# Kernel tuning notes

Measured on AMD Instinct MI355X. Metric: run time of the kernel, lower is better.

Reference implementation:

```python
import jax, jax.numpy as jnp
import numpy as np
from jax import lax

B = 256

elu = jax.nn.elu

def conv2d(x, w, b=None, stride=1, pad=0):
    out = lax.conv_general_dilated(x, w, (stride, stride), [(pad, pad), (pad, pad)],
                                   dimension_numbers=('NCHW', 'OIHW', 'NCHW'))
    if b is not None:
        out = out + b[None, :, None, None]
    return out

def convT2d(x, w, b, stride, pad):
    k = w.shape[2]
    wt = jnp.flip(w, (2, 3)).transpose(1, 0, 2, 3)
    p = k - 1 - pad
    out = lax.conv_general_dilated(x, wt, (1, 1), [(p, p), (p, p)], lhs_dilation=(stride, stride),
                                   dimension_numbers=('NCHW', 'OIHW', 'NCHW'))
    return out + b[None, :, None, None]

def batchnorm(x, g, b, eps=1e-5):
    m = x.mean((0, 2, 3), keepdims=True)
    v = x.var((0, 2, 3), keepdims=True)
    return g[None, :, None, None] * (x - m) * lax.rsqrt(v + eps) + b[None, :, None, None]

def pool2(x, op):
    b, c, h, w = x.shape
    h2, w2 = (h // 2) * 2, (w // 2) * 2
    xr = x[:, :, :h2, :w2].reshape(b, c, h2 // 2, 2, w2 // 2, 2)
    return xr.max((3, 5)) if op == 'max' else xr.mean((3, 5))

def cubic(A, Bv, C, D, t):
    a = -0.5 * A + 1.5 * Bv - 1.5 * C + 0.5 * D
    b = A - 2.5 * Bv + 2.0 * C - 0.5 * D
    c = -0.5 * A + 0.5 * C
    return ((a * t + b) * t + c) * t + Bv

def bicubic_resize(x, nh, nw):
    b, h, w, c = x.shape
    fy = jnp.arange(nh, dtype=x.dtype) * ((h - 1) / max(nh - 1, 1))
    fx = jnp.arange(nw, dtype=x.dtype) * ((w - 1) / max(nw - 1, 1))
    y0 = jnp.floor(fy).astype(jnp.int32); ty = (fy - y0)[None, :, None, None]
    x0 = jnp.floor(fx).astype(jnp.int32); tx = (fx - x0)[None, None, :, None]
    rows = []
    for ky in (-1, 0, 1, 2):
        r = x[:, jnp.clip(y0 + ky, 0, h - 1)]
        cols = [r[:, :, jnp.clip(x0 + kx, 0, w - 1)] for kx in (-1, 0, 1, 2)]
        rows.append(cubic(cols[0], cols[1], cols[2], cols[3], tx))
    return cubic(rows[0], rows[1], rows[2], rows[3], ty)

def warp_bicubic(V, img):
    b, h, w, _ = V.shape
    gx = jnp.linspace(-1., 1., w)[None, None, :] + V[..., 0]
    gy = jnp.linspace(-1., 1., h)[None, :, None] + V[..., 1]
    ix = (gx + 1) * (w - 1) / 2
    iy = (gy + 1) * (h - 1) / 2
    x0 = jnp.floor(ix); y0 = jnp.floor(iy)
    tx = ix - x0; ty = iy - y0
    flat = img.reshape(b, h * w)
    def g(ky, kx):
        yi = jnp.clip(y0 + ky, 0, h - 1).astype(jnp.int32)
        xi = jnp.clip(x0 + kx, 0, w - 1).astype(jnp.int32)
        return jnp.take_along_axis(flat, (yi * w + xi).reshape(b, -1), 1).reshape(b, h, w)
    rows = [cubic(g(ky, -1), g(ky, 0), g(ky, 1), g(ky, 2), tx) for ky in (-1, 0, 1, 2)]
    return cubic(rows[0], rows[1], rows[2], rows[3], ty)[..., None]

def grid_sample_bilinear(img, gx, gy):
    b, h, w = img.shape
    ix = ((gx + 1) * w - 1) / 2
    iy = ((gy + 1) * h - 1) / 2
    x0 = jnp.floor(ix); y0 = jnp.floor(iy)
    tx = ix - x0; ty = iy - y0
    flat = img.reshape(b, h * w)
    def g(xi, yi):
        valid = (xi >= 0) & (xi <= w - 1) & (yi >= 0) & (yi <= h - 1)
        xc = jnp.clip(xi, 0, w - 1).astype(jnp.int32)
        yc = jnp.clip(yi, 0, h - 1).astype(jnp.int32)
        v = jnp.take_along_axis(flat, (yc * w + xc).reshape(b, -1), 1).reshape(b, h, w)
        return jnp.where(valid, v, 0.)
    return ((1 - tx) * (1 - ty) * g(x0, y0) + tx * (1 - ty) * g(x0 + 1, y0)
            + (1 - tx) * ty * g(x0, y0 + 1) + tx * ty * g(x0 + 1, y0 + 1))

def deform_conv(x, pw, pb, mw, mb, w):
    b, c, h, wd = x.shape
    N = 9
    off = conv2d(x, pw, pb, pad=1)
    m = jax.nn.sigmoid(conv2d(x, mw, mb, pad=1))
    r = jnp.array([-1., 0., 1.], x.dtype)
    pnx, pny = jnp.meshgrid(r, r, indexing='ij')
    pnx = pnx.reshape(-1); pny = pny.reshape(-1)
    p0x = jnp.arange(1, h + 1, dtype=x.dtype)[None, None, :, None]
    p0y = jnp.arange(1, wd + 1, dtype=x.dtype)[None, None, None, :]
    Hp, Wp = h + 2, wd + 2
    px = jnp.clip(p0x + pnx[None, :, None, None] + off[:, :N], 0, Hp - 1)
    py = jnp.clip(p0y + pny[None, :, None, None] + off[:, N:], 0, Wp - 1)
    fx = jnp.floor(px); fy = jnp.floor(py)
    x0 = jnp.clip(fx, 0, Hp - 1); y0 = jnp.clip(fy, 0, Wp - 1)
    x1_ = jnp.clip(fx + 1, 0, Hp - 1); y1_ = jnp.clip(fy + 1, 0, Wp - 1)
    g_lt = (1 + (x0 - px)) * (1 + (y0 - py))
    g_rb = (1 - (x1_ - px)) * (1 - (y1_ - py))
    g_lb = (1 + (x0 - px)) * (1 - (y1_ - py))
    g_rt = (1 - (x1_ - px)) * (1 + (y0 - py))
    xpad = jnp.pad(x, ((0, 0), (0, 0), (1, 1), (1, 1))).reshape(b, c, Hp * Wp)
    def gather(qx, qy):
        idx = (qx * Wp + qy).astype(jnp.int32).reshape(b, 1, -1)
        v = jnp.take_along_axis(xpad, jnp.broadcast_to(idx, (b, c, idx.shape[-1])), 2)
        return v.reshape(b, c, N, h, wd)
    v = (g_lt[:, None] * gather(x0, y0) + g_rb[:, None] * gather(x1_, y1_)
         + g_lb[:, None] * gather(x0, y1_) + g_rt[:, None] * gather(x1_, y0))
    v = v * m[:, None]
    v = v.reshape(b, c, 3, 3, h, wd).transpose(0, 1, 4, 2, 5, 3).reshape(b, c, h * 3, wd * 3)
    return conv2d(v, w, stride=3)

def stn(x, lw1, lb1, lw2, lb2, fw1, fb1, fw2, fb2):
    xs = jax.nn.relu(pool2(conv2d(x, lw1, lb1), 'max'))
    xs = jax.nn.relu(pool2(conv2d(xs, lw2, lb2), 'max'))
    xs = xs.reshape(xs.shape[0], -1)
    th = jax.nn.relu(xs @ fw1.T + fb1) @ fw2.T + fb2
    theta = th.reshape(-1, 2, 3)
    b, _, h, w = x.shape
    ys = (2 * jnp.arange(h) + 1) / h - 1
    xn = (2 * jnp.arange(w) + 1) / w - 1
    GX, GY = jnp.meshgrid(xn, ys, indexing='xy')
    gx = theta[:, 0, 0][:, None, None] * GX + theta[:, 0, 1][:, None, None] * GY + theta[:, 0, 2][:, None, None]
    gy = theta[:, 1, 0][:, None, None] * GX + theta[:, 1, 1][:, None, None] * GY + theta[:, 1, 2][:, None, None]
    warped = grid_sample_bilinear(x[:, 0], gx, gy)
    return jnp.stack([warped, x[:, 1]], 1)

def _forward(x1, loc1_w, loc1_b, loc2_w, loc2_b, fc1_w, fc1_b, fc2_w, fc2_b, conv1_w, conv1_b, bn1_g, bn1_b, dc2_pw, dc2_pb, dc2_mw, dc2_mb, dc2_w, bn2_g, bn2_b, conv3_w, conv3_b, bn3_g, bn3_b, dc41_pw, dc41_pb, dc41_mw, dc41_mb, dc41_w, bn41_g, bn41_b, conv4_w, conv4_b, conv4m_w, conv4m_b, conv3m_w, conv3m_b, conv2m_w, conv2m_b, conv1m_w, conv1m_b):
    _ = stn(x1, loc1_w, loc1_b, loc2_w, loc2_b, fc1_w, fc1_b, fc2_w, fc2_b)
    x = elu(batchnorm(conv2d(x1, conv1_w, conv1_b, pad=1), bn1_g, bn1_b))
    x = pool2(x, 'avg')
    x = elu(batchnorm(deform_conv(x, dc2_pw, dc2_pb, dc2_mw, dc2_mb, dc2_w), bn2_g, bn2_b))
    x = elu(batchnorm(conv2d(x, conv3_w, conv3_b, pad=1), bn3_g, bn3_b))
    x = pool2(x, 'avg')
    x = elu(batchnorm(deform_conv(x, dc41_pw, dc41_pb, dc41_mw, dc41_mb, dc41_w), bn41_g, bn41_b))
    x = conv2d(x, conv4_w, conv4_b, pad=1)
    dvf = bicubic_resize(x.transpose(0, 3, 2, 1), 7, 7)
    x = dvf.transpose(0, 3, 2, 1)
    x = convT2d(x, conv4m_w, conv4m_b, 2, 1)
    x = convT2d(x, conv3m_w, conv3m_b, 1, 0)
    x = elu(x)
    x = elu(convT2d(x, conv2m_w, conv2m_b, 2, 1))
    x = elu(convT2d(x, conv1m_w, conv1m_b, 1, 1))
    Vt = bicubic_resize(x.transpose(0, 3, 2, 1), 28, 28)
    return warp_bicubic(Vt, x1[:, 0])

def setup_inputs() -> dict:
    key = jax.random.key(0)
    ks = iter(jax.random.split(key, 64))
    def rn(shape, s=0.05):
        return jax.random.normal(next(ks), shape, jnp.float32) * s
    return dict(
        x1=jax.random.normal(next(ks), (B, 2, 28, 28), jnp.float32),
        loc1_w=rn((8, 2, 7, 7)), loc1_b=rn((8,)),
        loc2_w=rn((10, 8, 5, 5)), loc2_b=rn((10,)),
        fc1_w=rn((32, 90)), fc1_b=rn((32,)),
        fc2_w=jnp.zeros((6, 32), jnp.float32),
        fc2_b=jnp.array([1., 0., 0., 0., 1., 0.], jnp.float32),
        conv1_w=rn((64, 2, 3, 3)), conv1_b=rn((64,)),
        bn1_g=jnp.ones((64,), jnp.float32), bn1_b=jnp.zeros((64,), jnp.float32),
        dc2_pw=rn((18, 64, 3, 3)), dc2_pb=rn((18,)),
        dc2_mw=rn((9, 64, 3, 3)), dc2_mb=rn((9,)),
        dc2_w=rn((128, 64, 3, 3)),
        bn2_g=jnp.ones((128,), jnp.float32), bn2_b=jnp.zeros((128,), jnp.float32),
        conv3_w=rn((128, 128, 3, 3)), conv3_b=rn((128,)),
        bn3_g=jnp.ones((128,), jnp.float32), bn3_b=jnp.zeros((128,), jnp.float32),
        dc41_pw=rn((18, 128, 3, 3)), dc41_pb=rn((18,)),
        dc41_mw=rn((9, 128, 3, 3)), dc41_mb=rn((9,)),
        dc41_w=rn((64, 128, 3, 3)),
        bn41_g=jnp.ones((64,), jnp.float32), bn41_b=jnp.zeros((64,), jnp.float32),
        conv4_w=rn((2, 64, 3, 3)), conv4_b=rn((2,)),
        conv4m_w=rn((2, 128, 3, 3)), conv4m_b=rn((128,)),
        conv3m_w=rn((128, 64, 3, 3)), conv3m_b=rn((64,)),
        conv2m_w=rn((64, 32, 3, 3)), conv2m_b=rn((32,)),
        conv1m_w=rn((32, 2, 2, 2)), conv1m_b=rn((2,)),
    )

def reference(x1, loc1_w, loc1_b, loc2_w, loc2_b, fc1_w, fc1_b, fc2_w, fc2_b, conv1_w, conv1_b, bn1_g, bn1_b, dc2_pw, dc2_pb, dc2_mw, dc2_mb, dc2_w, bn2_g, bn2_b, conv3_w, conv3_b, bn3_g, bn3_b, dc41_pw, dc41_pb, dc41_mw, dc41_mb, dc41_w, bn41_g, bn41_b, conv4_w, conv4_b, conv4m_w, conv4m_b, conv3m_w, conv3m_b, conv2m_w, conv2m_b, conv1m_w, conv1m_b):
    return _forward(x1, loc1_w, loc1_b, loc2_w, loc2_b, fc1_w, fc1_b, fc2_w, fc2_b, conv1_w, conv1_b, bn1_g, bn1_b, dc2_pw, dc2_pb, dc2_mw, dc2_mb, dc2_w, bn2_g, bn2_b, conv3_w, conv3_b, bn3_g, bn3_b, dc41_pw, dc41_pb, dc41_mw, dc41_mb, dc41_w, bn41_g, bn41_b, conv4_w, conv4_b, conv4m_w, conv4m_b, conv3m_w, conv3m_b, conv2m_w, conv2m_b, conv1m_w, conv1m_b)
```

## Files before the change

### kernel.cpp

```cpp
#include <hip/hip_runtime.h>
#include <hip/hip_bf16.h>
#include <hip/hip_fp16.h>

__device__ __forceinline__ float eluf(float x){ return x > 0.f ? x : expm1f(x); }

typedef __attribute__((ext_vector_type(8))) short bf16x8;
typedef __attribute__((ext_vector_type(8))) _Float16 f16x8;
typedef __attribute__((ext_vector_type(4))) float f32x4;

__device__ __forceinline__ unsigned int bf16r(float f){
  unsigned int u = __float_as_uint(f);
  return (u + 0x7FFFu + ((u >> 16) & 1u)) >> 16;
}

__device__ __forceinline__ unsigned short f16b(float f){
  __half h = __float2half(f);
  return __half_as_ushort(h);
}

constexpr int pad_stride(int wp){
  int s = (wp + 3) & ~3;
  return (s % 8 == 0) ? s + 4 : s;
}

__global__ __launch_bounds__(256)
void conv1_stats(const float* __restrict__ in, const float* __restrict__ w,
                 const float* __restrict__ bias, float* __restrict__ part)
{
  constexpr int WPL = pad_stride(30);
  __shared__ __align__(16) float img[2][30*WPL];
  __shared__ float wl[2][8*9];
  __shared__ float sred[8], qred[8];
  const int b = blockIdx.x, gy = blockIdx.y, o0 = gy*8, t = threadIdx.x;
  const int ol = t & 7, y = t >> 3;
  if (t < 8){ sred[t] = 0.f; qred[t] = 0.f; }
  for (int idx = t; idx < 2*30*WPL; idx += 256) ((float*)img)[idx] = 0.f;
  __syncthreads();
  for (int idx = t; idx < 2*784; idx += 256){
    int cl = idx/784, r = idx%784;
    img[cl][(r/28 + 1)*WPL + (r%28) + 1] = in[((long long)b*2)*784 + idx];
  }
  if (t < 144){
    int cl = t/72, r = t%72;
    wl[cl][r] = w[(((long long)(o0 + r/9))*2 + cl)*9 + (r%9)];
  }
  __syncthreads();
  const bool active = (y < 28);
  float acc[28];
  #pragma unroll
  for (int x = 0; x < 28; x++) acc[x] = 0.f;
  if (active){
    for (int cl = 0; cl < 2; cl++){
      #pragma unroll
      for (int ky = 0; ky < 3; ky++){
        const float* row = &img[cl][(y+ky)*WPL];
        float rin[30];
        #pragma unroll
        for (int q = 0; q < 7; q++){
          float4 v = ((const float4*)row)[q];
          rin[4*q+0]=v.x; rin[4*q+1]=v.y; rin[4*q+2]=v.z; rin[4*q+3]=v.w;
        }
        rin[28] = row[28]; rin[29] = row[29];
        #pragma unroll
        for (int kx = 0; kx < 3; kx++){
          float wv = wl[cl][ol*9 + ky*3 + kx];
          #pragma unroll
          for (int x = 0; x < 28; x++) acc[x] += wv * rin[x+kx];
        }
      }
    }
  }
  const int og = o0 + ol;
  float sv = 0.f, qv = 0.f;
  if (active){
    float bv = bias[og];
    #pragma unroll
    for (int x = 0; x < 28; x++){
      float v = acc[x] + bv;
      sv += v; qv += v*v;
    }
  }
  #pragma unroll
  for (int d = 32; d >= 8; d >>= 1){
    sv += __shfl_down(sv, d);
    qv += __shfl_down(qv, d);
  }
  if ((t & 63) < 8){ atomicAdd(&sred[ol], sv); atomicAdd(&qred[ol], qv); }
  __syncthreads();
  if (t < 8){
    float* pp = part + ((long long)(b*8 + gy))*16;
    pp[t]     = sred[t];
    pp[t + 8] = qred[t];
  }
}

__global__ __launch_bounds__(256)
void conv1_reduce(const float* __restrict__ part, float* __restrict__ sum, float* __restrict__ sq)
{
  __shared__ float ss[256], qq[256];
  const int t = threadIdx.x;
  const int c = t & 63, seg = t >> 6;
  const int gy = c >> 3, ol = c & 7;
  float sv = 0.f, qv = 0.f;
  for (int b = seg*64; b < seg*64 + 64; b++){
    const float* pp = part + ((long long)(b*8 + gy))*16;
    sv += pp[ol];
    qv += pp[ol + 8];
  }
  ss[t] = sv; qq[t] = qv;
  __syncthreads();
  if (t < 64){
    sum[c] = ss[t] + ss[t+64] + ss[t+128] + ss[t+192];
    sq[c]  = qq[t] + qq[t+64] + qq[t+128] + qq[t+192];
  }
}

__global__ __launch_bounds__(256)
void conv1_pool(const float* __restrict__ in, const float* __restrict__ w,
                const float* __restrict__ bias, const float* __restrict__ g,
                const float* __restrict__ bb, const float* __restrict__ sum,
                const float* __restrict__ sq, float* __restrict__ out)
{
  constexpr int WPL = pad_stride(30);
  constexpr int PST = 197;
  __shared__ __align__(16) float img[2][30*WPL];
  __shared__ float wl[2][16*9];
  __shared__ float pout[16*PST];
  const int b = blockIdx.x, o0 = blockIdx.y*16, t = threadIdx.x;
  const int ol = t & 15, yp = t >> 4;
  for (int idx = t; idx < 2*30*WPL; idx += 256) ((float*)img)[idx] = 0.f;
  __syncthreads();
  for (int idx = t; idx < 2*784; idx += 256){
    int cl = idx/784, r = idx%784;
    img[cl][(r/28 + 1)*WPL + (r%28) + 1] = in[((long long)b*2)*784 + idx];
  }
  for (int idx = t; idx < 288; idx += 256){
    int cl = idx/144, r = idx%144;
    wl[cl][r] = w[(((long long)(o0 + r/9))*2 + cl)*9 + (r%9)];
  }
  __syncthreads();
  if (yp < 14){
    float accA[28], accB[28];
    #pragma unroll
    for (int x = 0; x < 28; x++){ accA[x] = 0.f; accB[x] = 0.f; }
    for (int cl = 0; cl < 2; cl++){
      #pragma unroll
      for (int ky = 0; ky < 3; ky++){
        const float* rowA = &img[cl][(2*yp+ky)*WPL];
        const float* rowB = rowA + WPL;
        float ra[30], rb[30];
        #pragma unroll
        for (int q = 0; q < 7; q++){
          float4 va = ((const float4*)rowA)[q];
          ra[4*q+0]=va.x; ra[4*q+1]=va.y; ra[4*q+2]=va.z; ra[4*q+3]=va.w;
          float4 vb = ((const float4*)rowB)[q];
          rb[4*q+0]=vb.x; rb[4*q+1]=vb.y; rb[4*q+2]=vb.z; rb[4*q+3]=vb.w;
        }
        ra[28]=rowA[28]; ra[29]=rowA[29];
        rb[28]=rowB[28]; rb[29]=rowB[29];
        #pragma unroll
        for (int kx = 0; kx < 3; kx++){
          float wv = wl[cl][ol*9 + ky*3 + kx];
          #pragma unroll
          for (int x = 0; x < 28; x++){
            accA[x] += wv * ra[x+kx];
            accB[x] += wv * rb[x+kx];
          }
        }
      }
    }
    const int og = o0 + ol;
    const float bv = bias[og];
    const float invN = 1.f/200704.f;
    float mean = sum[og]*invN;
    float var  = sq[og]*invN - mean*mean;
    float sc = g[og] * rsqrtf(var + 1e-5f);
    float sh = bb[og] - mean*sc;
    float* po = &pout[ol*PST + yp*14];
    #pragma unroll
    for (int xp = 0; xp < 14; xp++){
      float acc = eluf(sc*(accA[2*xp]   + bv) + sh);
      acc      += eluf(sc*(accA[2*xp+1] + bv) + sh);
      acc      += eluf(sc*(accB[2*xp]   + bv) + sh);
      acc      += eluf(sc*(accB[2*xp+1] + bv) + sh);
      po[xp] = acc * 0.25f;
    }
  }
  __syncthreads();
  float* gbase = out + ((long long)b*64 + o0)*196;
  for (int idx = t; idx < 3136; idx += 256)
    gbase[idx] = pout[(idx/196)*PST + idx%196];
}

template<int CIN,int H,int W,int NZ>
__global__ __launch_bounds__(256)
void offmask_tiled(const float* __restrict__ in, const float* __restrict__ pw,
                   const float* __restrict__ pb, const float* __restrict__ mw,
                   const float* __restrict__ mb, float* __restrict__ om)
{
  constexpr int Hz  = H/NZ;
  constexpr int HP  = Hz + 2;
  constexpr int WP  = W + 2;
  constexpr int WPL = pad_stride(WP);
  __shared__ __align__(16) float img[CIN*HP*WPL];
  const int b = blockIdx.x;
  const int z = blockIdx.y;
  const int t = threadIdx.x;
  for (int i = t; i < CIN*HP*WPL; i += 256) img[i] = 0.f;
  __syncthreads();
  const int base = z*Hz - 1;
  const int gy0  = (base < 0) ? 0 : base;
  const int gy1  = (z*Hz + Hz + 1 > H) ? H : z*Hz + Hz + 1;
  const int nrows = gy1 - gy0;
  for (int i = t; i < CIN*nrows*W; i += 256){
    int x = i % W; int r = i / W;
    int row = r % nrows; int c = r / nrows;
    int gy = gy0 + row;
    img[(c*HP + (gy - base))*WPL + (x+1)] = in[((long long)b*CIN + c)*(H*W) + gy*W + x];
  }
  __syncthreads();
  const int o  = t & 31;
  const int yl = t >> 5;
  const int y  = z*Hz + yl;
  if (o < 27 && yl < Hz && y < H){
    float acc[W];
    #pragma unroll
    for (int x = 0; x < W; x++) acc[x] = 0.f;
    const float* wsrc = (o < 18) ? (pw + (long long)o*CIN*9) : (mw + (long long)(o-18)*CIN*9);
    for (int c = 0; c < CIN; c++){
      const float* wc = wsrc + c*9;
      float4 wa = *(const float4*)wc;
      float4 wbv = *(const float4*)(wc+4);
      float w8 = wc[8];
      const float* rm = &img[(c*HP + yl  )*WPL];
      const float* r0 = &img[(c*HP + yl+1)*WPL];
      const float* rp = &img[(c*HP + yl+2)*WPL];
      #pragma unroll
      for (int x = 0; x < W; x++){
        acc[x] += wa.x*rm[x] + wa.y*rm[x+1] + wa.z*rm[x+2]
                + wa.w*r0[x] + wbv.x*r0[x+1] + wbv.y*r0[x+2]
                + wbv.z*rp[x] + wbv.w*rp[x+1] + w8*rp[x+2];
      }
    }
    float bv = (o < 18) ? pb[o] : mb[o-18];
    float* po = om + (((long long)b*27 + o)*H + y)*W;
    #pragma unroll
    for (int x = 0; x < W; x++){
      float v = acc[x] + bv;
      if (o >= 18) v = 1.f/(1.f + expf(-v));
      po[x] = v;
    }
  }
}

__global__ __launch_bounds__(256)
void conv4_tiled(const float* __restrict__ in, const float* __restrict__ w,
                 const float* __restrict__ bias, float* __restrict__ out)
{
  __shared__ __align__(16) float img[64*9*12];
  __shared__ float wl[1152];
  const int b = blockIdx.x, t = threadIdx.x;
  for (int i = t; i < 64*108; i += 256) img[i] = 0.f;
  __syncthreads();
  for (int i = t; i < 64*49; i += 256){
    int px = i % 49, c = i / 49;
    img[(c*9 + px/7 + 1)*12 + (px%7) + 1] = in[((long long)b*64 + c)*49 + px];
  }
  for (int i = t; i < 1152; i += 256) wl[i] = w[i];
  __syncthreads();
  const int o  = t >> 7;
  const int px = t & 127;
  if (px < 49){
    int y = px/7, x = px%7;
    float acc = bias[o];
    const float* wo = &wl[o*576];
    for (int c = 0; c < 64; c++){
      const float* rm = &img[(c*9 + y)*12 + x];
      const float* r0 = rm + 12;
      const float* rp = rm + 24;
      const float* wc = wo + c*9;
      acc += wc[0]*rm[0]+wc[1]*rm[1]+wc[2]*rm[2]
           + wc[3]*r0[0]+wc[4]*r0[1]+wc[5]*r0[2]
           + wc[6]*rp[0]+wc[7]*rp[1]+wc[8]*rp[2];
    }
    out[((long long)b*2 + o)*49 + px] = acc;
  }
}

__global__ void wconv3_bf16_kernel(const float* __restrict__ w, unsigned short* __restrict__ wb)
{
  int idx = blockIdx.x*256 + threadIdx.x;
  if (idx >= 147456) return;
  int kk = idx >> 14;
  int r  = idx & 16383;
  int o  = r >> 7, c = r & 127;
  wb[idx] = (unsigned short)bf16r(w[((long long)o*128 + c)*9 + kk]);
}

__global__ void bn2_pack_kernel(const float* __restrict__ a2, const float* __restrict__ g,
                                const float* __restrict__ bb, const float* __restrict__ sum,
                                const float* __restrict__ sq, unsigned int* __restrict__ a2b)
{
  int idx = blockIdx.x*256 + threadIdx.x;
  if (idx >= 4194304) return;
  int c2 = idx & 31; int r = idx >> 5;
  int hp = r & 255; r >>= 8;
  int ch = r & 1; int b = r >> 1;
  int row = hp >> 4, col = hp & 15;
  unsigned val = 0u;
  if (row >= 1 && row <= 14 && col >= 1 && col <= 14){
    int px = (row-1)*14 + (col-1);
    int c = ch*64 + 2*c2;
    const float invN = 1.f/50176.f;
    float m0 = sum[c]*invN,     m1 = sum[c+1]*invN;
    float v0 = sq[c]*invN - m0*m0, v1 = sq[c+1]*invN - m1*m1;
    float sc0 = g[c]*rsqrtf(v0 + 1e-5f), sc1 = g[c+1]*rsqrtf(v1 + 1e-5f);
    float sh0 = bb[c] - m0*sc0, sh1 = bb[c+1] - m1*sc1;
    float x0 = a2[((long long)b*128 + c)*196 + px];
    float x1 = a2[((long long)b*128 + c + 1)*196 + px];
    float e0 = eluf(sc0*x0 + sh0), e1 = eluf(sc1*x1 + sh1);
    val = bf16r(e0) | (bf16r(e1) << 16);
  }
  a2b[idx] = val;
}

__global__ __launch_bounds__(256)
void conv3_mfma2(const unsigned short* __restrict__ a2b, const unsigned short* __restrict__ wb,
                 const float* __restrict__ bias, float* __restrict__ out,
                 float* __restrict__ sum, float* __restrict__ sq)
{
  constexpr int RS = 72;
  __shared__ __align__(16) unsigned short img[256*RS];
  __shared__ float sred[64], qred[64];
  const int b  = blockIdx.x;
  const int o0 = blockIdx.y * 64;
  const int t  = threadIdx.x;
  const int lane = t & 63, wv = t >> 6;
  const int l15 = lane & 15, q = lane >> 4;
  const int ntile = (wv == 0) ? 4 : 3;
  if (t < 64){ sred[t] = 0.f; qred[t] = 0.f; }
  int rbase[4];
  #pragma unroll
  for (int ti = 0; ti < 4; ti++){
    int px = (wv + ti*4)*16 + l15;
    int pxe = px < 196 ? px : 195;
    rbase[ti] = (pxe/14)*16 + (pxe%14);
  }
  f32x4 acc[4][4];
  #pragma unroll
  for (int og = 0; og < 4; og++)
    #pragma unroll
    for (int ti = 0; ti < 4; ti++) acc[og][ti] = (f32x4){0.f,0.f,0.f,0.f};
  for (int ch = 0; ch < 2; ch++){
    __syncthreads();
    const unsigned short* src = a2b + ((long long)(b*2 + ch))*16384;
    for (int it = t; it < 2048; it += 256){
      int r = it >> 3, j = it & 7;
      uint4 v = *(const uint4*)(src + r*64 + j*8);
      *(uint4*)&img[r*RS + j*8] = v;
    }
    __syncthreads();
    #pragma unroll
    for (int kk = 0; kk < 9; kk++){
      int dh = (kk/3)*16 + (kk%3);
      #pragma unroll
      for (int ks = 0; ks < 2; ks++){
        bf16x8 bf[4];
        #pragma unroll
        for (int ti = 0; ti < 4; ti++)
          if (ti < ntile)
            bf[ti] = *(const bf16x8*)&img[(rbase[ti]+dh)*RS + ks*32 + q*8];
        #pragma unroll
        for (int og = 0; og < 4; og++){
          const unsigned short* wp = wb + (((long long)kk*128 + o0 + og*16 + l15)*128 + ch*64 + ks*32 + q*8);
          bf16x8 af = *(const bf16x8*)wp;
          #pragma unroll
          for (int ti = 0; ti < 4; ti++)
            if (ti < ntile)
              acc[og][ti] = __builtin_amdgcn_mfma_f32_16x16x32_bf16(af, bf[ti], acc[og][ti], 0, 0, 0);
        }
      }
    }
  }
  float svl[4][4], qvl[4][4];
  #pragma unroll
  for (int og = 0; og < 4; og++)
    #pragma unroll
    for (int r = 0; r < 4; r++){ svl[og][r] = 0.f; qvl[og][r] = 0.f; }
  #pragma unroll
  for (int og = 0; og < 4; og++){
    #pragma unroll
    for (int ti = 0; ti < 4; ti++){
      if (ti < ntile){
        int px = (wv + ti*4)*16 + l15;
        if (px < 196){
          #pragma unroll
          for (int r = 0; r < 4; r++){
            int o = o0 + og*16 + q*4 + r;
            float v = acc[og][ti][r] + bias[o];
            out[((long long)b*128 + o)*196 + px] = v;
            svl[og][r] += v; qvl[og][r] += v*v;
          }
        }
      }
    }
  }
  #pragma unroll
  for (int og = 0; og < 4; og++)
    #pragma unroll
    for (int r = 0; r < 4; r++)
      #pragma unroll
      for (int m = 1; m < 16; m <<= 1){
        svl[og][r] += __shfl_xor(svl[og][r], m);
        qvl[og][r] += __shfl_xor(qvl[og][r], m);
      }
  if (l15 == 0){
    #pragma unroll
    for (int og = 0; og < 4; og++)
      #pragma unroll
      for (int r = 0; r < 4; r++){
        atomicAdd(&sred[og*16 + q*4 + r], svl[og][r]);
        atomicAdd(&qred[og*16 + q*4 + r], qvl[og][r]);
      }
  }
  __syncthreads();
  if (t < 64){ atomicAdd(&sum[o0 + t], sred[t]); atomicAdd(&sq[o0 + t], qred[t]); }
}

template<int HIN,int WIN,int CIN,int COUT,bool DO_ELU>
__global__ __launch_bounds__(256)
void convt_s2_tiled(const float* __restrict__ in, const float* __restrict__ w,
                    const float* __restrict__ bias, float* __restrict__ out)
{
  constexpr int HOUT = 2*HIN - 1, WOUT = 2*WIN - 1;
  constexpr int RS = 20;
  __shared__ __align__(16) float img[17*RS];
  __shared__ float wl[16][10];
  const int b  = blockIdx.x;
  const int o0 = blockIdx.y * 16;
  const int t  = threadIdx.x;
  const int ol = t & 15, yb = t >> 4;
  for (int idx = t; idx < 17*RS; idx += 256) img[idx] = 0.f;
  float accA[WOUT], accB[WOUT];
  #pragma unroll
  for (int x = 0; x < WOUT; x++){ accA[x] = 0.f; accB[x] = 0.f; }
  for (int c = 0; c < CIN; c++){
    __syncthreads();
    for (int idx = t; idx < HIN*WIN; idx += 256)
      img[(idx/WIN)*RS + idx%WIN] = in[((long long)b*CIN + c)*HIN*WIN + idx];
    if (t < 144)
      wl[t/9][t%9] = w[(((long long)c*COUT + o0 + t/9)*3 + (t%9)/3)*3 + (t%9)%3];
    __syncthreads();
    float ru[16], rd[16];
    #pragma unroll
    for (int q = 0; q < 4; q++){
      float4 va = ((const float4*)&img[yb*RS])[q];
      ru[4*q+0]=va.x; ru[4*q+1]=va.y; ru[4*q+2]=va.z; ru[4*q+3]=va.w;
      float4 vb = ((const float4*)&img[(yb+1)*RS])[q];
      rd[4*q+0]=vb.x; rd[4*q+1]=vb.y; rd[4*q+2]=vb.z; rd[4*q+3]=vb.w;
    }
    float w00=wl[ol][0], w01=wl[ol][1], w02=wl[ol][2];
    float w10=wl[ol][3], w11=wl[ol][4], w12=wl[ol][5];
    float w20=wl[ol][6], w21=wl[ol][7], w22=wl[ol][8];
    #pragma unroll
    for (int v = 0; v < WIN; v++){
      accA[2*v] += w11*ru[v];
      accB[2*v] += w21*ru[v] + w01*rd[v];
    }
    #pragma unroll
    for (int v = 0; v < WIN-1; v++){
      accA[2*v+1] += w12*ru[v] + w10*ru[v+1];
      accB[2*v+1] += w22*ru[v] + w20*ru[v+1] + w02*rd[v] + w00*rd[v+1];
    }
  }
  const int og = o0 + ol;
  const float bv = bias[og];
  const int yA = 2*yb, yB = 2*yb + 1;
  if (yA < HOUT){
    float* po = out + (((long long)b*COUT + og)*HOUT + yA)*WOUT;
    #pragma unroll
    for (int x = 0; x < WOUT; x++){ float v = accA[x] + bv; po[x] = DO_ELU ? eluf(v) : v; }
  }
  if (yB < HOUT){
    float* po = out + (((long long)b*COUT + og)*HOUT + yB)*WOUT;
    #pragma unroll
    for (int x = 0; x < WOUT; x++){ float v = accB[x] + bv; po[x] = DO_ELU ? eluf(v) : v; }
  }
}

__global__ void wdeform_f16_kernel(const float* __restrict__ w, unsigned short* __restrict__ wf,
                                   int CIN, int COUT)
{
  int n = (CIN/16)*COUT*160;
  int idx = blockIdx.x*256 + threadIdx.x;
  if (idx >= n) return;
  int ch = idx / (COUT*160);
  int r  = idx % (COUT*160);
  int o  = r / 160, k = r % 160;
  unsigned short h = 0;
  if (k < 144){
    int kk = k >> 4, cp = k & 15;
    h = f16b(w[((long long)o*CIN + ch*16 + cp)*9 + kk]);
  }
  wf[idx] = h;
}

__global__ void wconvt3m_split_kernel(const float* __restrict__ w, unsigned short* __restrict__ whi,
                                      unsigned short* __restrict__ wlo)
{
  int idx = blockIdx.x*256 + threadIdx.x;
  if (idx >= 73728) return;
  int kk = idx / 8192;
  int r  = idx % 8192;
  int o  = r >> 7, c = r & 127;
  int ky = kk/3, kx = kk%3;
  float v = w[(((long long)c*64 + o)*3 + (2-ky))*3 + (2-kx)];
  unsigned hu = bf16r(v);
  float res = v - __uint_as_float(hu << 16);
  whi[idx] = (unsigned short)hu;
  wlo[idx] = (unsigned short)bf16r(res);
}

__global__ void wconvt2m_split_kernel(const float* __restrict__ w, unsigned short* __restrict__ whi,
                                      unsigned short* __restrict__ wlo)
{
  int idx = blockIdx.x*256 + threadIdx.x;
  if (idx >= 18432) return;
  int kk = idx / 2048;
  int r  = idx % 2048;
  int o  = r >> 6, c = r & 63;
  float v = w[((long long)c*32 + o)*9 + kk];
  unsigned hu = bf16r(v);
  float res = v - __uint_as_float(hu << 16);
  whi[idx] = (unsigned short)hu;
  wlo[idx] = (unsigned short)bf16r(res);
}

template<int CIN,int COUT,int H,int W,int PXT,int NT,int NPT,int OTW>
__global__ __launch_bounds__(256)
void deform_mfma(const float* __restrict__ x, const float* __restrict__ om,
                 const unsigned short* __restrict__ wf,
                 float* __restrict__ out, float* __restrict__ sum, float* __restrict__ sq)
{
  constexpr int HW  = H*W;
  constexpr int CC  = 16;
  constexpr int NCH = CIN/CC;
  constexpr int GS  = 168;
  constexpr int KP  = 160;
  __shared__ __align__(16) float simg[CC*HW];
  __shared__ __align__(16) unsigned short Gf[PXT*GS];
  __shared__ __align__(16) float kwv[PXT*9*4];
  __shared__ __align__(4)  unsigned char kidx[PXT*9*4];
  const int tile = blockIdx.x % NT;
  const int b    = blockIdx.x / NT;
  const int t    = threadIdx.x;
  const int lane = t & 63, wv = t >> 6;
  const int l15  = lane & 15, q = lane >> 4;
  const int Hp = H + 2, Wp = W + 2;
  for (int idx = t; idx < PXT*16; idx += 256){
    int px = idx >> 4, k = 144 + (idx & 15);
    Gf[px*GS + k] = 0;
  }
  for (int it = t; it < PXT*9; it += 256){
    int px = it / 9, kk = it % 9;
    int p = tile*PXT + px;
    float w0=0.f,w1=0.f,w2=0.f,w3=0.f;
    int i0=0,i1=0,i2=0,i3=0;
    if (p < HW){
      int i = p / W, j = p % W;
      long long base = ((long long)b*27)*HW + p;
      float offx = om[base + (long long)kk*HW];
      float offy = om[base + (long long)(9+kk)*HW];
      float mk   = om[base + (long long)(18+kk)*HW];
      float pnx = (float)(kk/3) - 1.f;
      float pny = (float)(kk%3) - 1.f;
      float px_ = fminf(fmaxf((float)(i+1) + pnx + offx, 0.f), (float)(Hp-1));
      float py_ = fminf(fmaxf((float)(j+1) + pny + offy, 0.f), (float)(Wp-1));
      float fx = floorf(px_), fy = floorf(py_);
      float x0 = fmaxf(fx, 0.f), y0 = fmaxf(fy, 0.f);
      float x1c = fminf(fx + 1.f, (float)(Hp-1));
      float y1c = fminf(fy + 1.f, (float)(Wp-1));
      float glt = (1.f + (x0 - px_)) * (1.f + (y0 - py_));
      float grb = (1.f - (x1c - px_)) * (1.f - (y1c - py_));
      float glb = (1.f + (x0 - px_)) * (1.f - (y1c - py_));
      float grt = (1.f - (x1c - px_)) * (1.f + (y0 - py_));
      int ax0=(int)x0, ay0=(int)y0, ax1=(int)x1c, ay1=(int)y1c;
      if (ax0>=1 && ax0<=H && ay0>=1 && ay0<=W){ w0 = glt*mk; i0 = (ax0-1)*W + (ay0-1); }
      if (ax1>=1 && ax1<=H && ay1>=1 && ay1<=W){ w1 = grb*mk; i1 = (ax1-1)*W + (ay1-1); }
      if (ax0>=1 && ax0<=H && ay1>=1 && ay1<=W){ w2 = glb*mk; i2 = (ax0-1)*W + (ay1-1); }
      if (ax1>=1 && ax1<=H && ay0>=1 && ay0<=W){ w3 = grt*mk; i3 = (ax1-1)*W + (ay0-1); }
    }
    int b4 = it*4;
    kwv[b4+0]=w0; kwv[b4+1]=w1; kwv[b4+2]=w2; kwv[b4+3]=w3;
    kidx[b4+0]=(unsigned char)i0; kidx[b4+1]=(unsigned char)i1;
    kidx[b4+2]=(unsigned char)i2; kidx[b4+3]=(unsigned char)i3;
  }
  int grow[NPT];
  #pragma unroll
  for (int pt = 0; pt < NPT; pt++){
    int p = pt*16 + l15; if (p > PXT-1) p = PXT-1;
    grow[pt] = p*GS;
  }
  f32x4 acc[OTW][NPT];
  #pragma unroll
  for (int ot = 0; ot < OTW; ot++)
    #pragma unroll
    for (int pt = 0; pt < NPT; pt++) acc[ot][pt] = (f32x4){0.f,0.f,0.f,0.f};

  for (int ch = 0; ch < NCH; ch++){
    __syncthreads();
    {
      const float4* src = (const float4*)&x[((long long)b*CIN + ch*CC)*HW];
      for (int idx = t; idx < (CC*HW)/4; idx += 256)
        ((float4*)simg)[idx] = src[idx];
    }
    __syncthreads();
    for (int it = t; it < PXT*9*4; it += 256){
      int c4 = it & 3; int r = it >> 2;
      int kk = r % 9, px = r / 9;
      int b4 = (px*9 + kk)*4;
      float4 wv4 = *(const float4*)&kwv[b4];
      uchar4 id4 = *(const uchar4*)&kidx[b4];
      const float* pl = &simg[(4*c4)*HW];
      unsigned long long uo = 0ull;
      #pragma unroll
      for (int u = 0; u < 4; u++){
        const float* im = pl + u*HW;
        float v = wv4.x*im[id4.x] + wv4.y*im[id4.y] + wv4.z*im[id4.z] + wv4.w*im[id4.w];
        uo |= (unsigned long long)f16b(v) << (16*u);
      }
      *(unsigned long long*)&Gf[px*GS + kk*16 + 4*c4] = uo;
    }
    __syncthreads();
    const unsigned short* wh = wf + (long long)ch*COUT*KP;
    #pragma unroll
    for (int st = 0; st < 5; st++){
      f16x8 bh[NPT];
      #pragma unroll
      for (int pt = 0; pt < NPT; pt++)
        bh[pt] = *(const f16x8*)&Gf[grow[pt] + st*32 + q*8];
      #pragma unroll
      for (int ot = 0; ot < OTW; ot++){
        int o = (wv*OTW + ot)*16 + l15;
        f16x8 ah = *(const f16x8*)&wh[o*KP + st*32 + q*8];
        #pragma unroll
        for (int pt = 0; pt < NPT; pt++)
          acc[ot][pt] = __builtin_amdgcn_mfma_f32_16x16x32_f16(ah, bh[pt], acc[ot][pt], 0, 0, 0);
      }
    }
  }
  float* sred = kwv;
  float* qred = kwv + COUT;
  float sv[OTW][4], qv[OTW][4];
  #pragma unroll
  for (int ot = 0; ot < OTW; ot++)
    #pragma unroll
    for (int r = 0; r < 4; r++){ sv[ot][r] = 0.f; qv[ot][r] = 0.f; }
  #pragma unroll
  for (int ot = 0; ot < OTW; ot++){
    #pragma unroll
    for (int pt = 0; pt < NPT; pt++){
      int p = pt*16 + l15;
      int gp = tile*PXT + p;
      bool ok = (p < PXT) && (gp < HW);
      #pragma unroll
      for (int r = 0; r < 4; r++){
        if (ok){
          int o = (wv*OTW + ot)*16 + q*4 + r;
          float v = acc[ot][pt][r];
          out[((long long)b*COUT + o)*HW + gp] = v;
          sv[ot][r] += v; qv[ot][r] += v*v;
        }
      }
    }
  }
  #pragma unroll
  for (int ot = 0; ot < OTW; ot++)
    #pragma unroll
    for (int r = 0; r < 4; r++)
      #pragma unroll
      for (int m = 1; m < 16; m <<= 1){
        sv[ot][r] += __shfl_xor(sv[ot][r], m);
        qv[ot][r] += __shfl_xor(qv[ot][r], m);
      }
  __syncthreads();
  if (t < COUT){ sred[t] = 0.f; qred[t] = 0.f; }
  __syncthreads();
  if (l15 == 0){
    #pragma unroll
    for (int ot = 0; ot < OTW; ot++)
      #pragma unroll
      for (int r = 0; r < 4; r++){
        int o = (wv*OTW + ot)*16 + q*4 + r;
        atomicAdd(&sred[o], sv[ot][r]);
        atomicAdd(&qred[o], qv[ot][r]);
      }
  }
  __syncthreads();
  if (t < COUT){ atomicAdd(&sum[t], sred[t]); atomicAdd(&sq[t], qred[t]); }
}

__global__ __launch_bounds__(256)
void convt3m_mfma(const float* __restrict__ in, const unsigned short* __restrict__ wbhi,
                  const unsigned short* __restrict__ wblo, const float* __restrict__ bias,
                  float* __restrict__ out)
{
  constexpr int RS = 40;
  __shared__ __align__(16) unsigned short gh[289*RS];
  __shared__ __align__(16) unsigned short gl[289*RS];
  const int b  = blockIdx.x;
  const int zt = blockIdx.y;
  const int t  = threadIdx.x;
  const int lane = t & 63, wv = t >> 6;
  const int l15 = lane & 15, q = lane >> 4;
  const int og0 = (wv & 1)*2;
  const int tb  = zt*8 + (wv >> 1)*4;
  const int ntl = (zt == 0) ? 4 : ((wv >> 1) ? 3 : 4);
  f32x4 acc[2][4];
  #pragma unroll
  for (int ot = 0; ot < 2; ot++)
    #pragma unroll
    for (int ti = 0; ti < 4; ti++) acc[ot][ti] = (f32x4){0.f,0.f,0.f,0.f};
  {
    unsigned* zg = (unsigned*)gh; unsigned* zl = (unsigned*)gl;
    for (int idx = t; idx < 289*RS/2; idx += 256){ zg[idx] = 0u; zl[idx] = 0u; }
  }
  for (int cq = 0; cq < 4; cq++){
    __syncthreads();
    for (int idx = t; idx < 16*169; idx += 256){
      int c2 = idx / 169, px = idx % 169;
      int c = 2*c2;
      const float* ip = in + ((long long)b*128 + cq*32 + c)*169 + px;
      float f0 = ip[0];
      float f1 = ip[169];
      unsigned h0 = bf16r(f0); unsigned l0 = bf16r(f0 - __uint_as_float(h0<<16));
      unsigned h1 = bf16r(f1); unsigned l1 = bf16r(f1 - __uint_as_float(h1<<16));
      int hp = (px/13 + 2)*17 + (px%13) + 2;
      *(unsigned*)&gh[hp*RS + c] = h0 | (h1<<16);
      *(unsigned*)&gl[hp*RS + c] = l0 | (l1<<16);
    }
    __syncthreads();
    #pragma unroll
    for (int kk = 0; kk < 9; kk++){
      const long long wo = ((long long)kk*64)*128 + (long long)cq*32 + q*8;
      bf16x8 ah0 = *(const bf16x8*)&wbhi[wo + (long long)(og0*16 + l15)*128];
      bf16x8 al0 = *(const bf16x8*)&wblo[wo + (long long)(og0*16 + l15)*128];
      bf16x8 ah1 = *(const bf16x8*)&wbhi[wo + (long long)((og0+1)*16 + l15)*128];
      bf16x8 al1 = *(const bf16x8*)&wblo[wo + (long long)((og0+1)*16 + l15)*128];
      #pragma unroll
      for (int ti = 0; ti < 4; ti++){
        if (ti < ntl){
          int px = (tb + ti)*16 + l15;
          int pxe = px < 225 ? px : 224;
          int hp = (pxe/15 + kk/3)*17 + (pxe%15) + (kk%3);
          bf16x8 bh = *(const bf16x8*)&gh[hp*RS + q*8];
          bf16x8 bl = *(const bf16x8*)&gl[hp*RS + q*8];
          acc[0][ti] = __builtin_amdgcn_mfma_f32_16x16x32_bf16(ah0, bh, acc[0][ti], 0, 0, 0);
          acc[0][ti] = __builtin_amdgcn_mfma_f32_16x16x32_bf16(ah0, bl, acc[0][ti], 0, 0, 0);
          acc[0][ti] = __builtin_amdgcn_mfma_f32_16x16x32_bf16(al0, bh, acc[0][ti], 0, 0, 0);
          acc[1][ti] = __builtin_amdgcn_mfma_f32_16x16x32_bf16(ah1, bh, acc[1][ti], 0, 0, 0);
          acc[1][ti] = __builtin_amdgcn_mfma_f32_16x16x32_bf16(ah1, bl, acc[1][ti], 0, 0, 0);
          acc[1][ti] = __builtin_amdgcn_mfma_f32_16x16x32_bf16(al1, bh, acc[1][ti], 0, 0, 0);
        }
      }
    }
  }
  #pragma unroll
  for (int ot = 0; ot < 2; ot++){
    #pragma unroll
    for (int ti = 0; ti < 4; ti++){
      if (ti < ntl){
        int px = (tb + ti)*16 + l15;
        if (px < 225){
          #pragma unroll
          for (int r = 0; r < 4; r++){
            int o = (og0 + ot)*16 + q*4 + r;
            float v = eluf(acc[ot][ti][r] + bias[o]);
            out[((long long)b*64 + o)*225 + px] = v;
          }
        }
      }
    }
  }
}

__global__ __launch_bounds__(256)
void convt2m_mfma(const float* __restrict__ in, const unsigned short* __restrict__ wbhi,
                  const unsigned short* __restrict__ wblo, const float* __restrict__ bias,
                  float* __restrict__ out)
{
  constexpr int RS = 40;
  __shared__ __align__(16) unsigned short gh[256*RS];
  __shared__ __align__(16) unsigned short gl[256*RS];
  const int b  = blockIdx.x;
  const int z  = blockIdx.y;
  const int t  = threadIdx.x;
  const int lane = t & 63, wv = t >> 6;
  const int l15 = lane & 15, q = lane >> 4;
  const int g = z*4 + wv;
  f32x4 acc[2][7];
  #pragma unroll
  for (int og = 0; og < 2; og++)
    #pragma unroll
    for (int i = 0; i < 7; i++) acc[og][i] = (f32x4){0.f,0.f,0.f,0.f};
  {
    unsigned* zg = (unsigned*)gh; unsigned* zl = (unsigned*)gl;
    for (int idx = t; idx < 256*RS/2; idx += 256){ zg[idx] = 0u; zl[idx] = 0u; }
  }
  for (int cq = 0; cq < 2; cq++){
    __syncthreads();
    for (int idx = t; idx < 16*225; idx += 256){
      int c2 = idx / 225, px = idx % 225;
      int c = 2*c2;
      const float* ip = in + ((long long)b*64 + cq*32 + c)*225 + px;
      float f0 = ip[0];
      float f1 = ip[225];
      unsigned h0 = bf16r(f0); unsigned l0 = bf16r(f0 - __uint_as_float(h0<<16));
      unsigned h1 = bf16r(f1); unsigned l1 = bf16r(f1 - __uint_as_float(h1<<16));
      int hp = (px/15)*16 + (px%15);
      *(unsigned*)&gh[hp*RS + c] = h0 | (h1<<16);
      *(unsigned*)&gl[hp*RS + c] = l0 | (l1<<16);
    }
    __syncthreads();
    #pragma unroll
    for (int i = 0; i < 7; i++){
      int T = g + i*8;
      int cls, tt;
      if (T < 15){ cls = 0; tt = T; }
      else if (T < 29){ cls = 1; tt = T - 15; }
      else if (T < 43){ cls = 2; tt = T - 29; }
      else { cls = 3; tt = T - 43; }
      int np = (cls == 0) ? 225 : (cls == 3) ? 196 : 210;
      int Wd = (cls == 0 || cls == 2) ? 15 : 14;
      int p = tt*16 + l15;
      int pe = p < np ? p : np - 1;
      int m = pe / Wd, n = pe % Wd;
      int hp0 = m*16 + n;
      int ry = (cls < 2) ? 1 : 2;
      int rx = ((cls & 1) == 0) ? 1 : 2;
      for (int jy = 0; jy < ry; jy++){
        int wky = (cls < 2) ? 1 : (jy == 0 ? 2 : 0);
        int shy = (cls < 2) ? 0 : (jy == 0 ? 0 : 16);
        for (int jx = 0; jx < rx; jx++){
          int wkx = ((cls & 1) == 0) ? 1 : (jx == 0 ? 2 : 0);
          int shx = ((cls & 1) == 0) ? 0 : (jx == 0 ? 0 : 1);
          int kk = wky*3 + wkx;
          int hp = hp0 + shy + shx;
          bf16x8 bh = *(const bf16x8*)&gh[hp*RS + q*8];
          bf16x8 bl = *(const bf16x8*)&gl[hp*RS + q*8];
          const long long wo = ((long long)kk*32)*64 + cq*32 + q*8;
          bf16x8 ah0 = *(const bf16x8*)&wbhi[wo + (long long)l15*64];
          bf16x8 al0 = *(const bf16x8*)&wblo[wo + (long long)l15*64];
          bf16x8 ah1 = *(const bf16x8*)&wbhi[wo + (long long)(16 + l15)*64];
          bf16x8 al1 = *(const bf16x8*)&wblo[wo + (long long)(16 + l15)*64];
          acc[0][i] = __builtin_amdgcn_mfma_f32_16x16x32_bf16(ah0, bh, acc[0][i], 0, 0, 0);
          acc[0][i] = __builtin_amdgcn_mfma_f32_16x16x32_bf16(ah0, bl, acc[0][i], 0, 0, 0);
          acc[0][i] = __builtin_amdgcn_mfma_f32_16x16x32_bf16(al0, bh, acc[0][i], 0, 0, 0);
          acc[1][i] = __builtin_amdgcn_mfma_f32_16x16x32_bf16(ah1, bh, acc[1][i], 0, 0, 0);
          acc[1][i] = __builtin_amdgcn_mfma_f32_16x16x32_bf16(ah1, bl, acc[1][i], 0, 0, 0);
          acc[1][i] = __builtin_amdgcn_mfma_f32_16x16x32_bf16(al1, bh, acc[1][i], 0, 0, 0);
        }
      }
    }
  }
  #pragma unroll
  for (int i = 0; i < 7; i++){
    int T = g + i*8;
    int cls, tt;
    if (T < 15){ cls = 0; tt = T; }
    else if (T < 29){ cls = 1; tt = T - 15; }
    else if (T < 43){ cls = 2; tt = T - 29; }
    else { cls = 3; tt = T - 43; }
    int np = (cls == 0) ? 225 : (cls == 3) ? 196 : 210;
    int clsOff = (cls == 0) ? 0 : (cls == 1) ? 225 : (cls == 2) ? 435 : 645;
    int p = tt*16 + l15;
    if (p < np){
      #pragma unroll
      for (int og = 0; og < 2; og++){
        #pragma unroll
        for (int r = 0; r < 4; r++){
          int o = og*16 + q*4 + r;
          float v = eluf(acc[og][i][r] + bias[o]);
          out[((long long)b*32 + o)*841 + clsOff + p] = v;
        }
      }
    }
  }
}

__global__ __launch_bounds__(256)
void convt1m_lds_kernel(const float* __restrict__ in, const float* __restrict__ w,
                        const float* __restrict__ bias, float* __restrict__ out)
{
  __shared__ float simg[32*841];
  __shared__ float wl[256];
  const int b = blockIdx.x, t = threadIdx.x;
  for (int i = t; i < 32*841; i += 256) simg[i] = in[(long long)b*32*841 + i];
  if (t < 256) wl[t] = w[t];
  __syncthreads();
  const float* bsrc = simg;
  for (int i = t; i < 1568; i += 256){
    int x = i % 28; int r = i / 28;
    int y = r % 28; int o = r / 28;
    float acc = bias[o];
    #pragma unroll
    for (int ky = 0; ky < 2; ky++){
      int iy = y + ky;
      int wky = 1 - ky;
      #pragma unroll
      for (int kx = 0; kx < 2; kx++){
        int ix = x + kx;
        int wkx = 1 - kx;
        int cls = (iy & 1)*2 + (ix & 1);
        int Wd  = (ix & 1) ? 14 : 15;
        int off = ((cls == 0) ? 0 : (cls == 1) ? 225 : (cls == 2) ? 435 : 645)
                + (iy >> 1)*Wd + (ix >> 1);
        const float* ip = bsrc + off;
        for (int c = 0; c < 32; c++){
          acc += wl[((c*2 + o)*2 + wky)*2 + wkx] * ip[c*841];
        }
      }
    }
    out[(long long)b*1568 + i] = eluf(acc);
  }
}

__global__ void bn_elu_pool_kernel(const float* __restrict__ in, const float* __restrict__ g,
                                   const float* __restrict__ bb, const float* __restrict__ sum,
                                   const float* __restrict__ sq, float* __restrict__ out,
                                   int B, int C, int H, int W, float invN)
{
  int Ho = H/2, Wo = W/2;
  int idx = blockIdx.x*256 + threadIdx.x;
  int total = B*C*Ho*Wo;
  if (idx >= total) return;
  int x = idx % Wo; int t = idx / Wo;
  int y = t % Ho;   t /= Ho;
  int c = t % C;    int b = t / C;
  float mean = sum[c]*invN;
  float var  = sq[c]*invN - mean*mean;
  float sc = g[c] * rsqrtf(var + 1e-5f);
  float sh = bb[c] - mean*sc;
  const float* p = in + (long long)(b*C + c)*H*W;
  float acc = 0.f;
  #pragma unroll
  for (int dy = 0; dy < 2; dy++)
    #pragma unroll
    for (int dx = 0; dx < 2; dx++)
      acc += eluf(sc*p[(2*y+dy)*W + (2*x+dx)] + sh);
  out[idx] = acc * 0.25f;
}

__global__ void bn_elu_inplace_kernel(float* __restrict__ xio, const float* __restrict__ g,
                                      const float* __restrict__ bb, const float* __restrict__ sum,
                                      const float* __restrict__ sq, int C, int HW, float invN, int total)
{
  int idx = blockIdx.x*256 + threadIdx.x;
  if (idx >= total) return;
  int c = (idx / HW) % C;
  float mean = sum[c]*invN;
  float var  = sq[c]*invN - mean*mean;
  float sc = g[c] * rsqrtf(var + 1e-5f);
  float sh = bb[c] - mean*sc;
  xio[idx] = eluf(sc*xio[idx] + sh);
}

__device__ __forceinline__ float cubicf(float A, float Bv, float C, float D, float t){
  float a = -0.5f*A + 1.5f*Bv - 1.5f*C + 0.5f*D;
  float b =  A - 2.5f*Bv + 2.0f*C - 0.5f*D;
  float c = -0.5f*A + 0.5f*C;
  return ((a*t + b)*t + c)*t + Bv;
}

__global__ void warp_kernel(const float* __restrict__ V, const float* __restrict__ x1,
                            float* __restrict__ out, int B)
{
  int idx = blockIdx.x*256 + threadIdx.x;
  int total = B*784;
  if (idx >= total) return;
  int j = idx % 28; int t = idx / 28;
  int i = t % 28;   int b = t / 28;
  float v0 = V[((long long)b*2 + 0)*784 + j*28 + i];
  float v1 = V[((long long)b*2 + 1)*784 + j*28 + i];
  float gx = (-1.f + 2.f*(float)j/27.f) + v0;
  float gy = (-1.f + 2.f*(float)i/27.f) + v1;
  float ix = (gx + 1.f)*13.5f;
  float iy = (gy + 1.f)*13.5f;
  float x0 = floorf(ix), y0 = floorf(iy);
  float tx = ix - x0, ty = iy - y0;
  const float* img = x1 + (long long)b*2*784;
  float rows[4];
  #pragma unroll
  for (int ky = -1; ky <= 2; ky++){
    int yi = (int)fminf(fmaxf(y0 + (float)ky, 0.f), 27.f);
    float cv[4];
    #pragma unroll
    for (int kx = -1; kx <= 2; kx++){
      int xi = (int)fminf(fmaxf(x0 + (float)kx, 0.f), 27.f);
      cv[kx+1] = img[yi*28 + xi];
    }
    rows[ky+1] = cubicf(cv[0], cv[1], cv[2], cv[3], tx);
  }
  out[idx] = cubicf(rows[0], rows[1], rows[2], rows[3], ty);
}

extern "C" void kernel_launch(void* const* d_in, const int* in_sizes, int n_in,
                              void* d_out, int out_size, void* d_ws, size_t ws_size,
                              hipStream_t stream)
{
  const int B = 256;
  const float* x1      = (const float*)d_in[0];
  const float* conv1_w = (const float*)d_in[9];
  const float* conv1_b = (const float*)d_in[10];
  const float* bn1_g   = (const float*)d_in[11];
  const float* bn1_b   = (const float*)d_in[12];
  const float* dc2_pw  = (const float*)d_in[13];
  const float* dc2_pb  = (const float*)d_in[14];
  const float* dc2_mw  = (const float*)d_in[15];
  const float* dc2_mb  = (const float*)d_in[16];
  const float* dc2_w   = (const float*)d_in[17];
  const float* bn2_g   = (const float*)d_in[18];
  const float* bn2_b   = (const float*)d_in[19];
  const float* conv3_w = (const float*)d_in[20];
  const float* conv3_b = (const float*)d_in[21];
  const float* bn3_g   = (const float*)d_in[22];
  const float* bn3_b   = (const float*)d_in[23];
  const float* dc41_pw = (const float*)d_in[24];
  const float* dc41_pb = (const float*)d_in[25];
  const float* dc41_mw = (const float*)d_in[26];
  const float* dc41_mb = (const float*)d_in[27];
  const float* dc41_w  = (const float*)d_in[28];
  const float* bn41_g  = (const float*)d_in[29];
  const float* bn41_b  = (const float*)d_in[30];
  const float* conv4_w = (const float*)d_in[31];
  const float* conv4_b = (const float*)d_in[32];
  const float* conv4m_w= (const float*)d_in[33];
  const float* conv4m_b= (const float*)d_in[34];
  const float* conv3m_w= (const float*)d_in[35];
  const float* conv3m_b= (const float*)d_in[36];
  const float* conv2m_w= (const float*)d_in[37];
  const float* conv2m_b= (const float*)d_in[38];
  const float* conv1m_w= (const float*)d_in[39];
  const float* conv1m_b= (const float*)d_in[40];

  float* ws = (float*)d_ws;

  const long long AB = 1024;
  float* p1   = ws + AB;
  float* cpart= ws + AB;
  float* om2  = ws + AB + 3211264;
  float* a2   = ws + AB + 4566016;
  float* a3   = ws + AB + 10988544;
  float* p2   = ws + AB;
  float* om41 = ws + AB + 1605632;
  float* a41  = ws + AB + 1944320;
  float* a4   = ws + AB + 2747136;
  float* t4m  = ws + AB + 2772224;
  float* t3m  = ws + AB + 8310016;
  float* t2m  = ws + AB + 1048576;
  float* t1m  = ws + AB;
  unsigned int* a2b = (unsigned int*)(ws + AB);
  unsigned short* wb2f   = (unsigned short*)(ws + AB + 17411072);
  unsigned short* wb41f  = wb2f + 81920;
  unsigned short* wb3mhi = (unsigned short*)(ws + AB + 17705984);
  unsigned short* wb3mlo = wb3mhi + 73728;
  unsigned short* wb3 = (unsigned short*)(ws + AB + 17779712);
  unsigned short* wb2mhi = (unsigned short*)(ws + AB);
  unsigned short* wb2mlo = wb2mhi + 18432;

  float* s1  = ws + 0;   float* q1  = ws + 64;
  float* s2  = ws + 128; float* q2  = ws + 256;
  float* s3  = ws + 384; float* q3  = ws + 512;
  float* s41 = ws + 640; float* q41 = ws + 704;

  auto nb = [](long long n){ return (int)((n + 255)/256); };

  hipMemsetAsync(d_ws, 0, 4096, stream);

  wconv3_bf16_kernel<<<nb(147456), 256, 0, stream>>>(conv3_w, wb3);
  wdeform_f16_kernel<<<nb(81920), 256, 0, stream>>>(dc2_w,  wb2f,  64, 128);
  wdeform_f16_kernel<<<nb(81920), 256, 0, stream>>>(dc41_w, wb41f, 128, 64);
  wconvt3m_split_kernel<<<nb(73728), 256, 0, stream>>>(conv3m_w, wb3mhi, wb3mlo);

  conv1_stats<<<dim3(B,8), 256, 0, stream>>>(x1, conv1_w, conv1_b, cpart);
  conv1_reduce<<<1, 256, 0, stream>>>(cpart, s1, q1);
  conv1_pool<<<dim3(B,4), 256, 0, stream>>>(x1, conv1_w, conv1_b, bn1_g, bn1_b, s1, q1, p1);
  offmask_tiled<64,14,14,2><<<dim3(B,2), 256, 0, stream>>>(p1, dc2_pw, dc2_pb, dc2_mw, dc2_mb, om2);
  deform_mfma<64,128,14,14,49,4,4,2><<<dim3(B*4), 256, 0, stream>>>(p1, om2, wb2f, a2, s2, q2);
  bn2_pack_kernel<<<nb(4194304), 256, 0, stream>>>(a2, bn2_g, bn2_b, s2, q2, a2b);
  conv3_mfma2<<<dim3(B,2), 256, 0, stream>>>((const unsigned short*)a2b, wb3, conv3_b, a3, s3, q3);
  bn_elu_pool_kernel<<<nb((long long)B*128*49), 256, 0, stream>>>(a3, bn3_g, bn3_b, s3, q3, p2,
                                                                  B, 128, 14, 14, 1.f/50176.f);
  offmask_tiled<128,7,7,1><<<dim3(B,1), 256, 0, stream>>>(p2, dc41_pw, dc41_pb, dc41_mw, dc41_mb, om41);
  deform_mfma<128,64,7,7,13,4,1,1><<<dim3(B*4), 256, 0, stream>>>(p2, om41, wb41f, a41, s41, q41);
  bn_elu_inplace_kernel<<<nb((long long)B*64*49), 256, 0, stream>>>(a41, bn41_g, bn41_b, s41, q41,
                                                                    64, 49, 1.f/12544.f, B*64*49);
  wconvt2m_split_kernel<<<nb(18432), 256, 0, stream>>>(conv2m_w, wb2mhi, wb2mlo);
  conv4_tiled<<<B, 256, 0, stream>>>(a41, conv4_w, conv4_b, a4);
  convt_s2_tiled<7,7,2,128,false><<<dim3(B,8), 256, 0, stream>>>(a4, conv4m_w, conv4m_b, t4m);
  convt3m_mfma<<<dim3(B,2), 256, 0, stream>>>(t4m, wb3mhi, wb3mlo, conv3m_b, t3m);
  convt2m_mfma<<<dim3(B,2), 256, 0, stream>>>(t3m, wb2mhi, wb2mlo, conv2m_b, t2m);
  convt1m_lds_kernel<<<B, 256, 0, stream>>>(t2m, conv1m_w, conv1m_b, t1m);
  warp_kernel<<<nb((long long)B*784), 256, 0, stream>>>(t1m, x1, (float*)d_out, B);
}
```

Measured before the change: 682.9 us.

## Prefetch next channel chunk into registers and interleave channel-plane mapping in deform kernel

The deformable conv MFMA kernel now loads the next 16-channel input chunk from global memory into registers while the current chunk's bilinear gather and MFMA run, then stores it to shared memory at the top of the next iteration. The gather's channel mapping is changed so each thread group reads planes c4, c4+4, c4+8, c4+12, and the f16 weight packing is permuted to match. This aims to hide global load latency and spread LDS bank accesses, at the cost of extra registers for the staging buffer, which may reduce occupancy.

```diff
diff --git a/kernel.cpp b/kernel.cpp
--- a/kernel.cpp
+++ b/kernel.cpp
@@ -500,7 +500,8 @@
   unsigned short h = 0;
   if (k < 144){
     int kk = k >> 4, cp = k & 15;
-    h = f16b(w[((long long)o*CIN + ch*16 + cp)*9 + kk]);
+    int cl = (cp >> 2) + 4*(cp & 3);
+    h = f16b(w[((long long)o*CIN + ch*16 + cl)*9 + kk]);
   }
   wf[idx] = h;
 }
@@ -547,6 +548,8 @@
   constexpr int NCH = CIN/CC;
   constexpr int GS  = 168;
   constexpr int KP  = 160;
+  constexpr int NV4 = CC*HW/4;
+  constexpr int NPL = (NV4 + 255)/256;
   __shared__ __align__(16) float simg[CC*HW];
   __shared__ __align__(16) unsigned short Gf[PXT*GS];
   __shared__ __align__(16) float kwv[PXT*9*4];
@@ -557,6 +560,15 @@
   const int lane = t & 63, wv = t >> 6;
   const int l15  = lane & 15, q = lane >> 4;
   const int Hp = H + 2, Wp = W + 2;
+  float4 rstage[NPL];
+  {
+    const float4* src = (const float4*)&x[(long long)b*CIN*HW];
+    #pragma unroll
+    for (int k = 0; k < NPL; k++){
+      int i = t + k*256;
+      if (i < NV4) rstage[k] = src[i];
+    }
+  }
   for (int idx = t; idx < PXT*16; idx += 256){
     int px = idx >> 4, k = 144 + (idx & 15);
     Gf[px*GS + k] = 0;
@@ -609,23 +621,31 @@
 
   for (int ch = 0; ch < NCH; ch++){
     __syncthreads();
-    {
-      const float4* src = (const float4*)&x[((long long)b*CIN + ch*CC)*HW];
-      for (int idx = t; idx < (CC*HW)/4; idx += 256)
-        ((float4*)simg)[idx] = src[idx];
+    #pragma unroll
+    for (int k = 0; k < NPL; k++){
+      int i = t + k*256;
+      if (i < NV4) ((float4*)simg)[i] = rstage[k];
     }
     __syncthreads();
+    if (ch + 1 < NCH){
+      const float4* src = (const float4*)&x[((long long)b*CIN + (ch+1)*CC)*HW];
+      #pragma unroll
+      for (int k = 0; k < NPL; k++){
+        int i = t + k*256;
+        if (i < NV4) rstage[k] = src[i];
+      }
+    }
     for (int it = t; it < PXT*9*4; it += 256){
       int c4 = it & 3; int r = it >> 2;
       int kk = r % 9, px = r / 9;
       int b4 = (px*9 + kk)*4;
       float4 wv4 = *(const float4*)&kwv[b4];
       uchar4 id4 = *(const uchar4*)&kidx[b4];
-      const float* pl = &simg[(4*c4)*HW];
+      const float* pl = &simg[c4*HW];
       unsigned long long uo = 0ull;
       #pragma unroll
       for (int u = 0; u < 4; u++){
-        const float* im = pl + u*HW;
+        const float* im = pl + u*(4*HW);
         float v = wv4.x*im[id4.x] + wv4.y*im[id4.y] + wv4.z*im[id4.z] + wv4.w*im[id4.w];
         uo |= (unsigned long long)f16b(v) << (16*u);
       }
```

Result: no change. 687.1 us (+0.6%).
